# Optimization experiments

Hardware: AMD Instinct MI355X
Metric: run time of the kernel (lower is better)

Reference implementation:

```python
import jax, jax.numpy as jnp
import numpy as np

S, N, D, H = 1024, 8, 1024, 16
DK = D // H
SCALE = np.sqrt(DK).astype(np.float32)


def setup_inputs() -> dict:
    key = jax.random.key(0)
    ks = jax.random.split(key, 16)
    f32 = jnp.float32
    Qpoi = jax.random.normal(ks[0], (S, N, D), f32)
    Qsvi = jax.random.normal(ks[1], (S, N, D), f32)
    K = jax.random.normal(ks[2], (S, N, D), f32)
    V = jax.random.normal(ks[3], (S, N, D), f32)
    # padding mask: True = masked key; random valid lengths in [S//2, S]
    lengths = jax.random.randint(ks[4], (N,), S // 2, S + 1)
    key_padding_mask = jnp.arange(S)[None, :] >= lengths[:, None]  # [N, S] bool
    w = 0.02
    wq_poi_w = jax.random.normal(ks[5], (D, D), f32) * w
    wq_poi_b = jnp.zeros((D,), f32)
    wq_svi_w = jax.random.normal(ks[6], (D, D), f32) * w
    wq_svi_b = jnp.zeros((D,), f32)
    wk_w = jax.random.normal(ks[7], (D, D), f32) * w
    wk_b = jnp.zeros((D,), f32)
    wv_w = jax.random.normal(ks[8], (D, D), f32) * w
    wv_b = jnp.zeros((D,), f32)
    fc_w = jax.random.normal(ks[9], (D, D), f32) * w
    fc_b = jnp.zeros((D,), f32)
    return dict(Qpoi=Qpoi, Qsvi=Qsvi, K=K, V=V, key_padding_mask=key_padding_mask,
                wq_poi_w=wq_poi_w, wq_poi_b=wq_poi_b, wq_svi_w=wq_svi_w, wq_svi_b=wq_svi_b,
                wk_w=wk_w, wk_b=wk_b, wv_w=wv_w, wv_b=wv_b, fc_w=fc_w, fc_b=fc_b)


def _proj_heads(x, W, b):
    # x: [S, N, D] -> linear -> [N, H, S, DK]
    y = x @ W.T + b                      # [S, N, D]
    y = jnp.transpose(y, (1, 0, 2))      # [N, S, D]
    y = y.reshape(N, S, H, DK)
    return jnp.transpose(y, (0, 2, 1, 3))  # [N, H, S, DK]


def _attend(Qh, Kh, Vh, mask):
    # Qh,Kh,Vh: [N, H, S, DK]; mask: [N, S] bool (True = masked)
    scores = jnp.einsum('nhqd,nhkd->nhqk', Qh, Kh) / SCALE
    scores = jnp.where(mask[:, None, None, :], -jnp.inf, scores)
    attn = jax.nn.softmax(scores, axis=-1)  # dropout is identity in eval
    out = jnp.einsum('nhqk,nhkd->nhqd', attn, Vh)
    out = jnp.transpose(out, (0, 2, 1, 3)).reshape(N, S, D)  # [N, S, D]
    return out


def reference(Qpoi, Qsvi, K, V, key_padding_mask,
              wq_poi_w, wq_poi_b, wq_svi_w, wq_svi_b,
              wk_w, wk_b, wv_w, wv_b, fc_w, fc_b):
    Qp = _proj_heads(Qpoi, wq_poi_w, wq_poi_b)
    Qs = _proj_heads(Qsvi, wq_svi_w, wq_svi_b)
    Kh = _proj_heads(K, wk_w, wk_b)
    Vh = _proj_heads(V, wv_w, wv_b)
    poi = _attend(Qp, Kh, Vh, key_padding_mask)
    svi = _attend(Qs, Kh, Vh, key_padding_mask)
    poi_out = jnp.transpose(poi @ fc_w.T + fc_b, (1, 0, 2))  # [S, N, D]
    svi_out = jnp.transpose(svi @ fc_w.T + fc_b, (1, 0, 2))
    return (poi_out, svi_out)
```

## Files before the change

### kernel.cpp

```cpp
#include <hip/hip_runtime.h>

typedef unsigned short u16;
typedef unsigned int u32;
typedef short bf16x8 __attribute__((ext_vector_type(8)));
typedef float f32x4 __attribute__((ext_vector_type(4)));

__device__ __forceinline__ u16 f2bf(float f) {
  union { float f; u32 i; } v; v.f = f;
  u32 x = v.i;
  return (u16)((x + 0x7fffu + ((x >> 16) & 1u)) >> 16);
}

union Pack16 { u16 h[16]; float4 f4[2]; };

__device__ __forceinline__ void gld16(const u16* g, u16* l) {
  __builtin_amdgcn_global_load_lds((const __attribute__((address_space(1))) u32*)g,
                                   (__attribute__((address_space(3))) u32*)l, 16, 0, 0);
}

struct C2 { const float* s[2]; u16* d[2]; };
__global__ __launch_bounds__(256) void conv2_kernel(C2 c) {
  const int z = blockIdx.z;
  const size_t i = (size_t)blockIdx.x * 256 + threadIdx.x;
  const float4* s = (const float4*)c.s[z] + i * 2;
  float4 a = s[0], b = s[1];
  union { u16 h[8]; float4 f; } o;
  o.h[0] = f2bf(a.x); o.h[1] = f2bf(a.y); o.h[2] = f2bf(a.z); o.h[3] = f2bf(a.w);
  o.h[4] = f2bf(b.x); o.h[5] = f2bf(b.y); o.h[6] = f2bf(b.z); o.h[7] = f2bf(b.w);
  *(float4*)(c.d[z] + i * 8) = o.f;
}

struct W5 { const float* p[5]; };
__global__ __launch_bounds__(256) void conv_w_kernel(W5 w, u16* __restrict__ dst) {
  const int m = blockIdx.x >> 9;
  const size_t i = (size_t)(blockIdx.x & 511) * 256 + threadIdx.x;
  const float4* s = (const float4*)w.p[m] + i * 2;
  float4 a = s[0], b = s[1];
  union { u16 h[8]; float4 f; } o;
  o.h[0] = f2bf(a.x); o.h[1] = f2bf(a.y); o.h[2] = f2bf(a.z); o.h[3] = f2bf(a.w);
  o.h[4] = f2bf(b.x); o.h[5] = f2bf(b.y); o.h[6] = f2bf(b.z); o.h[7] = f2bf(b.w);
  *(float4*)(dst + ((size_t)m << 20) + i * 8) = o.f;
}

template<int ASRC>
__device__ __forceinline__ const u16* aAddr(const u16* A, int row, int k) {
  if constexpr (ASRC == 0) {
    return A + (size_t)row * 1024 + k;
  } else {
    const int n = row >> 10, s = row & 1023, h = k >> 6;
    return A + ((size_t)((n * 16 + h) * 1024 + s)) * 64 + (k & 63);
  }
}

struct GB { const void* A[2]; const void* W[2]; const float* bias[2]; void* out[2]; };

template<int MODEA, int MODEB, int ASRC, int WBF>
__global__ __launch_bounds__(256, 2) void gemm_bt(GB gb) {
  __shared__ __align__(16) u16 At[2][128 * 32];
  __shared__ __align__(16) u16 Bt[2][128 * 32];

  const int z = blockIdx.z;
  const u16* Ab = (const u16*)gb.A[z];
  const u16* Wb = (const u16*)gb.W[z];
  const float* bias = gb.bias[z];
  void* outv = gb.out[z];
  const int mode = z ? MODEB : MODEA;

  const int tid = threadIdx.x;
  const int lane = tid & 63, wave = tid >> 6;
  const int quad = lane >> 4, l16 = lane & 15;
  const int bm = blockIdx.y * 128, bn = blockIdx.x * 128;
  const int wm = (wave >> 1) * 64, wn = (wave & 1) * 64;

  const int r0 = wave * 32;
  const int lrow = lane >> 2;
  const int lk = (lane & 3) * 8;
  (void)lrow;

  const int srow = tid >> 1, scol = (tid & 1) * 16;

  f32x4 acc[4][4];
#pragma unroll
  for (int i = 0; i < 4; i++)
#pragma unroll
    for (int j = 0; j < 4; j++) acc[i][j] = (f32x4){0.f, 0.f, 0.f, 0.f};

  float4 wf[4];

  auto loadWf = [&](int k0) {
    const float* wp = (const float*)Wb + (size_t)(bn + srow) * 1024 + k0 + scol;
#pragma unroll
    for (int q = 0; q < 4; q++) wf[q] = ((const float4*)wp)[q];
  };
  auto stageA = [&](int b, int k0) {
    const int row = bm + r0 + (lane >> 2);
    gld16(aAddr<ASRC>(Ab, row, k0 + lk), At[b] + r0 * 32);
    gld16(aAddr<ASRC>(Ab, row + 16, k0 + lk), At[b] + (r0 + 16) * 32);
  };
  auto stageW = [&](int b, int k0) {
    if constexpr (WBF) {
      const int row = bn + r0 + (lane >> 2);
      gld16(Wb + (size_t)row * 1024 + k0 + lk, Bt[b] + r0 * 32);
      gld16(Wb + (size_t)(row + 16) * 1024 + k0 + lk, Bt[b] + (r0 + 16) * 32);
    } else {
      Pack16 pb;
#pragma unroll
      for (int q = 0; q < 4; q++) {
        pb.h[q * 4 + 0] = f2bf(wf[q].x);
        pb.h[q * 4 + 1] = f2bf(wf[q].y);
        pb.h[q * 4 + 2] = f2bf(wf[q].z);
        pb.h[q * 4 + 3] = f2bf(wf[q].w);
      }
      *(float4*)(Bt[b] + srow * 32 + scol) = pb.f4[0];
      *(float4*)(Bt[b] + srow * 32 + scol + 8) = pb.f4[1];
    }
  };

  if constexpr (!WBF) loadWf(0);
  stageA(0, 0);
  stageW(0, 0);
  if constexpr (!WBF) loadWf(32);

  for (int t = 0; t < 32; ++t) {
    const int cb = t & 1, nb = cb ^ 1;
    __syncthreads();
    if (t + 1 < 32) {
      stageA(nb, (t + 1) * 32);
      stageW(nb, (t + 1) * 32);
      if constexpr (!WBF) if (t + 2 < 32) loadWf((t + 2) * 32);
    }

    bf16x8 af[4], bfr[4];
#pragma unroll
    for (int mt = 0; mt < 4; mt++)
      af[mt] = *(const bf16x8*)(At[cb] + (wm + mt * 16 + l16) * 32 + quad * 8);
#pragma unroll
    for (int nt = 0; nt < 4; nt++)
      bfr[nt] = *(const bf16x8*)(Bt[cb] + (wn + nt * 16 + l16) * 32 + quad * 8);
#pragma unroll
    for (int mt = 0; mt < 4; mt++)
#pragma unroll
      for (int nt = 0; nt < 4; nt++)
        acc[mt][nt] = __builtin_amdgcn_mfma_f32_16x16x32_bf16(af[mt], bfr[nt], acc[mt][nt], 0, 0, 0);
  }

#pragma unroll
  for (int mt = 0; mt < 4; mt++) {
#pragma unroll
    for (int nt = 0; nt < 4; nt++) {
      const int col = bn + wn + nt * 16 + l16;
      const float bv = bias[col];
#pragma unroll
      for (int i = 0; i < 4; i++) {
        const int row = bm + wm + mt * 16 + quad * 4 + i;
        const float v = acc[mt][nt][i] + bv;
        if (mode == 0) {
          const int s = row >> 3, n = row & 7;
          const int h = col >> 6, dk = col & 63;
          ((u16*)outv)[(size_t)(((n * 16 + h) * 1024 + s) * 64 + dk)] = f2bf(v);
        } else if (mode == 1) {
          const int n = row >> 10, s = row & 1023;
          ((float*)outv)[(size_t)((s * 8 + n) * 1024 + col)] = v;
        } else {
          const int s = row >> 3, n = row & 7;
          const int h = col >> 6, dk = col & 63;
          ((u16*)outv)[(size_t)(((n * 16 + h) * 64 + dk) * 1024 + s)] = f2bf(v);
        }
      }
    }
  }
}

__global__ __launch_bounds__(256, 2) void attn2_kernel(const u16* __restrict__ Qs_g,
                                                       const u16* __restrict__ Qp_g,
                                                       const u16* __restrict__ K,
                                                       const u16* __restrict__ Vt_g,
                                                       const int* __restrict__ mask,
                                                       u16* __restrict__ OUTs,
                                                       u16* __restrict__ OUTp) {
  __shared__ __align__(16) u16 Ks[64 * 72];
  __shared__ __align__(16) u16 Vt[64 * 64];
  __shared__ __align__(16) u16 PsS[4 * 16 * 72];
  __shared__ __align__(16) u16 PsP[4 * 16 * 72];
  __shared__ float mbias[64];

  const int tid = threadIdx.x;
  const int lane = tid & 63, wave = tid >> 6;
  const int quad = lane >> 4, l16 = lane & 15;
  const int qt = blockIdx.x, nh = blockIdx.y;
  const int n = nh >> 4;
  const size_t base = (size_t)nh << 16;

  const int q0 = qt * 64 + wave * 16;
  bf16x8 qS0, qS1, qP0, qP1;
  {
    const u16* qp = Qs_g + base + (size_t)(q0 + l16) * 64 + quad * 8;
    qS0 = *(const bf16x8*)qp;
    qS1 = *(const bf16x8*)(qp + 32);
    const u16* qq = Qp_g + base + (size_t)(q0 + l16) * 64 + quad * 8;
    qP0 = *(const bf16x8*)qq;
    qP1 = *(const bf16x8*)(qq + 32);
  }

  float mS[4], mP[4];
  f32x4 oS[4], oP[4], lS, lP;
#pragma unroll
  for (int i = 0; i < 4; i++) { mS[i] = -1e30f; mP[i] = -1e30f; }
#pragma unroll
  for (int d = 0; d < 4; d++) { oS[d] = (f32x4){0.f, 0.f, 0.f, 0.f}; oP[d] = (f32x4){0.f, 0.f, 0.f, 0.f}; }
  lS = (f32x4){0.f, 0.f, 0.f, 0.f};
  lP = (f32x4){0.f, 0.f, 0.f, 0.f};

  bf16x8 vbOnes;
  {
    const short ob = (l16 == 0) ? (short)0x3F80 : (short)0;
#pragma unroll
    for (int j = 0; j < 8; j++) vbOnes[j] = ob;
  }

  const int sr = tid >> 2;
  const int sc = (tid & 3) * 16;
  const u16* kbase = K + base + (size_t)sr * 64 + sc;
  const u16* vbase = Vt_g + base + (size_t)sr * 1024 + sc;
  u16* vdst0 = Vt + sr * 64 + ((((sc >> 3) + 0) ^ (sr & 7)) << 3);
  u16* vdst1 = Vt + sr * 64 + ((((sc >> 3) + 1) ^ (sr & 7)) << 3);
  u16* pwS = PsS + wave * (16 * 72);
  u16* pwP = PsP + wave * (16 * 72);

  float4 kv0 = *(const float4*)(kbase);
  float4 kv1 = *(const float4*)(kbase + 8);
  float4 vv0 = *(const float4*)(vbase);
  float4 vv1 = *(const float4*)(vbase + 8);
  int mk = (tid < 64) ? mask[n * 1024 + tid] : 0;

  for (int kt = 0; kt < 16; kt++) {
    __syncthreads();
    *(float4*)(Ks + sr * 72 + sc) = kv0;
    *(float4*)(Ks + sr * 72 + sc + 8) = kv1;
    *(float4*)vdst0 = vv0;
    *(float4*)vdst1 = vv1;
    if (tid < 64) mbias[tid] = mk ? -1e30f : 0.0f;
    __syncthreads();

    if (kt + 1 < 16) {
      kv0 = *(const float4*)(kbase + (kt + 1) * 64 * 64);
      kv1 = *(const float4*)(kbase + (kt + 1) * 64 * 64 + 8);
      vv0 = *(const float4*)(vbase + (kt + 1) * 64);
      vv1 = *(const float4*)(vbase + (kt + 1) * 64 + 8);
      mk = (tid < 64) ? mask[n * 1024 + (kt + 1) * 64 + tid] : 0;
    }

    f32x4 sS[4], sP[4];
#pragma unroll
    for (int nt = 0; nt < 4; nt++) {
      bf16x8 b0 = *(const bf16x8*)(Ks + (nt * 16 + l16) * 72 + quad * 8);
      bf16x8 b1 = *(const bf16x8*)(Ks + (nt * 16 + l16) * 72 + 32 + quad * 8);
      f32x4 a = (f32x4){0.f, 0.f, 0.f, 0.f};
      a = __builtin_amdgcn_mfma_f32_16x16x32_bf16(qS0, b0, a, 0, 0, 0);
      a = __builtin_amdgcn_mfma_f32_16x16x32_bf16(qS1, b1, a, 0, 0, 0);
      sS[nt] = a;
      f32x4 c = (f32x4){0.f, 0.f, 0.f, 0.f};
      c = __builtin_amdgcn_mfma_f32_16x16x32_bf16(qP0, b0, c, 0, 0, 0);
      c = __builtin_amdgcn_mfma_f32_16x16x32_bf16(qP1, b1, c, 0, 0, 0);
      sP[nt] = c;
    }
    float mb[4];
#pragma unroll
    for (int nt = 0; nt < 4; nt++) mb[nt] = mbias[nt * 16 + l16];
#pragma unroll
    for (int nt = 0; nt < 4; nt++)
#pragma unroll
      for (int i = 0; i < 4; i++) {
        sS[nt][i] = sS[nt][i] * 0.125f + mb[nt];
        sP[nt][i] = sP[nt][i] * 0.125f + mb[nt];
      }

#pragma unroll
    for (int i = 0; i < 4; i++) {
      float m = fmaxf(fmaxf(sS[0][i], sS[1][i]), fmaxf(sS[2][i], sS[3][i]));
#pragma unroll
      for (int off = 1; off < 16; off <<= 1) m = fmaxf(m, __shfl_xor(m, off, 64));
      float mn = fmaxf(mS[i], m);
      float alpha = __expf(mS[i] - mn);
      mS[i] = mn;
#pragma unroll
      for (int d = 0; d < 4; d++) oS[d][i] *= alpha;
      lS[i] *= alpha;
    }
#pragma unroll
    for (int i = 0; i < 4; i++) {
      float m = fmaxf(fmaxf(sP[0][i], sP[1][i]), fmaxf(sP[2][i], sP[3][i]));
#pragma unroll
      for (int off = 1; off < 16; off <<= 1) m = fmaxf(m, __shfl_xor(m, off, 64));
      float mn = fmaxf(mP[i], m);
      float alpha = __expf(mP[i] - mn);
      mP[i] = mn;
#pragma unroll
      for (int d = 0; d < 4; d++) oP[d][i] *= alpha;
      lP[i] *= alpha;
    }
#pragma unroll
    for (int nt = 0; nt < 4; nt++)
#pragma unroll
      for (int i = 0; i < 4; i++) {
        pwS[(quad * 4 + i) * 72 + nt * 16 + l16] = f2bf(__expf(sS[nt][i] - mS[i]));
        pwP[(quad * 4 + i) * 72 + nt * 16 + l16] = f2bf(__expf(sP[nt][i] - mP[i]));
      }
    __syncthreads();

#pragma unroll
    for (int ks = 0; ks < 2; ks++) {
      bf16x8 paS = *(const bf16x8*)(pwS + l16 * 72 + ks * 32 + quad * 8);
      bf16x8 paP = *(const bf16x8*)(pwP + l16 * 72 + ks * 32 + quad * 8);
      lS = __builtin_amdgcn_mfma_f32_16x16x32_bf16(paS, vbOnes, lS, 0, 0, 0);
      lP = __builtin_amdgcn_mfma_f32_16x16x32_bf16(paP, vbOnes, lP, 0, 0, 0);
#pragma unroll
      for (int d = 0; d < 4; d++) {
        bf16x8 vb = *(const bf16x8*)(Vt + (d * 16 + l16) * 64 +
                                     (((ks * 4 + quad) ^ (l16 & 7)) << 3));
        oS[d] = __builtin_amdgcn_mfma_f32_16x16x32_bf16(paS, vb, oS[d], 0, 0, 0);
        oP[d] = __builtin_amdgcn_mfma_f32_16x16x32_bf16(paP, vb, oP[d], 0, 0, 0);
      }
    }
  }

#pragma unroll
  for (int i = 0; i < 4; i++) {
    const float lsv = __shfl(lS[i], lane & 48, 64);
    const float lpv = __shfl(lP[i], lane & 48, 64);
    const float invS = 1.0f / lsv;
    const float invP = 1.0f / lpv;
    const int q = q0 + quad * 4 + i;
    const size_t ob = base + (size_t)q * 64;
#pragma unroll
    for (int d = 0; d < 4; d++) {
      OUTs[ob + d * 16 + l16] = f2bf(oS[d][i] * invS);
      OUTp[ob + d * 16 + l16] = f2bf(oP[d][i] * invP);
    }
  }
}

extern "C" void kernel_launch(void* const* d_in, const int* in_sizes, int n_in,
                              void* d_out, int out_size, void* d_ws, size_t ws_size,
                              hipStream_t stream) {
  const float* Qpoi = (const float*)d_in[0];
  const float* Qsvi = (const float*)d_in[1];
  const float* Kin  = (const float*)d_in[2];
  const float* Vin  = (const float*)d_in[3];
  const int* mask   = (const int*)d_in[4];
  const float* wq_poi_w = (const float*)d_in[5];
  const float* wq_poi_b = (const float*)d_in[6];
  const float* wq_svi_w = (const float*)d_in[7];
  const float* wq_svi_b = (const float*)d_in[8];
  const float* wk_w = (const float*)d_in[9];
  const float* wk_b = (const float*)d_in[10];
  const float* wv_w = (const float*)d_in[11];
  const float* wv_b = (const float*)d_in[12];
  const float* fc_w = (const float*)d_in[13];
  const float* fc_b = (const float*)d_in[14];

  const size_t SZ = (size_t)8 * 16 * 1024 * 64;
  const size_t WBE = (size_t)5 << 20;
  u16* W0 = (u16*)d_ws;
  u16* W1 = W0 + SZ;
  u16* Wp = W1 + SZ;
  const bool haveWb = ws_size >= (2 * SZ + WBE) * sizeof(u16);

  float* Of = (float*)d_out;
  u16* R0 = (u16*)d_out;
  u16* R1 = R0 + SZ;
  u16* R2 = R0 + 2 * SZ;
  u16* R3 = R0 + 3 * SZ;

  dim3 bb(256, 1, 1);
  dim3 gg(8, 64, 2);
  dim3 ga(16, 128);
  dim3 gc(4096, 1, 2);

  if (haveWb) {
    W5 w5{{wk_w, wv_w, wq_svi_w, wq_poi_w, fc_w}};
    hipLaunchKernelGGL(conv_w_kernel, dim3(2560), bb, 0, stream, w5, Wp);
  }
  const u16* Wk  = Wp + ((size_t)0 << 20);
  const u16* Wv  = Wp + ((size_t)1 << 20);
  const u16* Wqs = Wp + ((size_t)2 << 20);
  const u16* Wqp = Wp + ((size_t)3 << 20);
  const u16* Wfc = Wp + ((size_t)4 << 20);

  {
    C2 c{{Kin, Vin}, {R0, R1}};
    hipLaunchKernelGGL(conv2_kernel, gc, bb, 0, stream, c);
    GB g{{R0, R1},
         {haveWb ? (const void*)Wk : (const void*)wk_w, haveWb ? (const void*)Wv : (const void*)wv_w},
         {wk_b, wv_b}, {(void*)W0, (void*)W1}};
    if (haveWb) hipLaunchKernelGGL((gemm_bt<0, 2, 0, 1>), gg, bb, 0, stream, g);
    else        hipLaunchKernelGGL((gemm_bt<0, 2, 0, 0>), gg, bb, 0, stream, g);
  }

  {
    C2 c{{Qsvi, Qpoi}, {R0, R1}};
    hipLaunchKernelGGL(conv2_kernel, gc, bb, 0, stream, c);
    GB g{{R0, R1},
         {haveWb ? (const void*)Wqs : (const void*)wq_svi_w, haveWb ? (const void*)Wqp : (const void*)wq_poi_w},
         {wq_svi_b, wq_poi_b}, {(void*)R2, (void*)R3}};
    if (haveWb) hipLaunchKernelGGL((gemm_bt<0, 0, 0, 1>), gg, bb, 0, stream, g);
    else        hipLaunchKernelGGL((gemm_bt<0, 0, 0, 0>), gg, bb, 0, stream, g);
  }

  hipLaunchKernelGGL(attn2_kernel, ga, bb, 0, stream,
                     (const u16*)R2, (const u16*)R3, (const u16*)W0, (const u16*)W1,
                     mask, R2, R3);

  hipMemcpyAsync(W0, R3, SZ * sizeof(u16), hipMemcpyDeviceToDevice, stream);
  hipMemcpyAsync(W1, R2, SZ * sizeof(u16), hipMemcpyDeviceToDevice, stream);
  {
    GB g{{W0, W1},
         {haveWb ? (const void*)Wfc : (const void*)fc_w, haveWb ? (const void*)Wfc : (const void*)fc_w},
         {fc_b, fc_b}, {(void*)Of, (void*)(Of + SZ)}};
    if (haveWb) hipLaunchKernelGGL((gemm_bt<1, 1, 1, 1>), gg, bb, 0, stream, g);
    else        hipLaunchKernelGGL((gemm_bt<1, 1, 1, 0>), gg, bb, 0, stream, g);
  }
}
```

Baseline: 572.2 us.

## Transpose score MFMA, lazy softmax rescale, packed bf16 P, drop ctx memcpys

The attention kernel now computes transposed score tiles (K as the A operand), so each lane holds a single query column. This turns the row max into two cross-quad shuffles. Rescaling of the running output is skipped unless the tile max exceeds the running max by more than 8, the row sum is accumulated in VALU instead of an extra ones-MFMA, and P is written to a swizzled LDS buffer with packed bf16 converts, dropping a __syncthreads. When workspace is large enough, attention writes its context into dedicated buffers so the two device-to-device memcpys before the output GEMM are avoided. The risks are a larger workspace requirement and possible fp32 headroom issues from the lazy rescale threshold.

Result: faster. 474.0 us (-17.2%).

```diff
diff --git a/kernel.cpp b/kernel.cpp
--- a/kernel.cpp
+++ b/kernel.cpp
@@ -9,6 +9,12 @@
   union { float f; u32 i; } v; v.f = f;
   u32 x = v.i;
   return (u16)((x + 0x7fffu + ((x >> 16) & 1u)) >> 16);
+}
+
+__device__ __forceinline__ u32 cvtpk_bf16(float a, float b) {
+  u32 r;
+  asm("v_cvt_pk_bf16_f32 %0, %1, %2" : "=v"(r) : "v"(a), "v"(b));
+  return r;
 }
 
 union Pack16 { u16 h[16]; float4 f4[2]; };
@@ -73,9 +79,7 @@
   const int wm = (wave >> 1) * 64, wn = (wave & 1) * 64;
 
   const int r0 = wave * 32;
-  const int lrow = lane >> 2;
   const int lk = (lane & 3) * 8;
-  (void)lrow;
 
   const int srow = tid >> 1, scol = (tid & 1) * 16;
 
@@ -180,8 +184,7 @@
                                                        u16* __restrict__ OUTp) {
   __shared__ __align__(16) u16 Ks[64 * 72];
   __shared__ __align__(16) u16 Vt[64 * 64];
-  __shared__ __align__(16) u16 PsS[4 * 16 * 72];
-  __shared__ __align__(16) u16 PsP[4 * 16 * 72];
+  __shared__ __align__(16) u16 Ps[4][2][1024];
   __shared__ float mbias[64];
 
   const int tid = threadIdx.x;
@@ -202,21 +205,10 @@
     qP1 = *(const bf16x8*)(qq + 32);
   }
 
-  float mS[4], mP[4];
-  f32x4 oS[4], oP[4], lS, lP;
-#pragma unroll
-  for (int i = 0; i < 4; i++) { mS[i] = -1e30f; mP[i] = -1e30f; }
+  float mS = -1e30f, mP = -1e30f, lS = 0.f, lP = 0.f;
+  f32x4 oS[4], oP[4];
 #pragma unroll
   for (int d = 0; d < 4; d++) { oS[d] = (f32x4){0.f, 0.f, 0.f, 0.f}; oP[d] = (f32x4){0.f, 0.f, 0.f, 0.f}; }
-  lS = (f32x4){0.f, 0.f, 0.f, 0.f};
-  lP = (f32x4){0.f, 0.f, 0.f, 0.f};
-
-  bf16x8 vbOnes;
-  {
-    const short ob = (l16 == 0) ? (short)0x3F80 : (short)0;
-#pragma unroll
-    for (int j = 0; j < 8; j++) vbOnes[j] = ob;
-  }
 
   const int sr = tid >> 2;
   const int sc = (tid & 3) * 16;
@@ -224,8 +216,8 @@
   const u16* vbase = Vt_g + base + (size_t)sr * 1024 + sc;
   u16* vdst0 = Vt + sr * 64 + ((((sc >> 3) + 0) ^ (sr & 7)) << 3);
   u16* vdst1 = Vt + sr * 64 + ((((sc >> 3) + 1) ^ (sr & 7)) << 3);
-  u16* pwS = PsS + wave * (16 * 72);
-  u16* pwP = PsP + wave * (16 * 72);
+  u16* psS = &Ps[wave][0][0];
+  u16* psP = &Ps[wave][1][0];
 
   float4 kv0 = *(const float4*)(kbase);
   float4 kv1 = *(const float4*)(kbase + 8);
@@ -256,64 +248,79 @@
       bf16x8 b0 = *(const bf16x8*)(Ks + (nt * 16 + l16) * 72 + quad * 8);
       bf16x8 b1 = *(const bf16x8*)(Ks + (nt * 16 + l16) * 72 + 32 + quad * 8);
       f32x4 a = (f32x4){0.f, 0.f, 0.f, 0.f};
-      a = __builtin_amdgcn_mfma_f32_16x16x32_bf16(qS0, b0, a, 0, 0, 0);
-      a = __builtin_amdgcn_mfma_f32_16x16x32_bf16(qS1, b1, a, 0, 0, 0);
+      a = __builtin_amdgcn_mfma_f32_16x16x32_bf16(b0, qS0, a, 0, 0, 0);
+      a = __builtin_amdgcn_mfma_f32_16x16x32_bf16(b1, qS1, a, 0, 0, 0);
       sS[nt] = a;
       f32x4 c = (f32x4){0.f, 0.f, 0.f, 0.f};
-      c = __builtin_amdgcn_mfma_f32_16x16x32_bf16(qP0, b0, c, 0, 0, 0);
-      c = __builtin_amdgcn_mfma_f32_16x16x32_bf16(qP1, b1, c, 0, 0, 0);
+      c = __builtin_amdgcn_mfma_f32_16x16x32_bf16(b0, qP0, c, 0, 0, 0);
+      c = __builtin_amdgcn_mfma_f32_16x16x32_bf16(b1, qP1, c, 0, 0, 0);
       sP[nt] = c;
     }
-    float mb[4];
-#pragma unroll
-    for (int nt = 0; nt < 4; nt++) mb[nt] = mbias[nt * 16 + l16];
 #pragma unroll
     for (int nt = 0; nt < 4; nt++)
 #pragma unroll
       for (int i = 0; i < 4; i++) {
-        sS[nt][i] = sS[nt][i] * 0.125f + mb[nt];
-        sP[nt][i] = sP[nt][i] * 0.125f + mb[nt];
+        const float mb = mbias[nt * 16 + quad * 4 + i];
+        sS[nt][i] = sS[nt][i] * 0.125f + mb;
+        sP[nt][i] = sP[nt][i] * 0.125f + mb;
       }
 
-#pragma unroll
-    for (int i = 0; i < 4; i++) {
-      float m = fmaxf(fmaxf(sS[0][i], sS[1][i]), fmaxf(sS[2][i], sS[3][i]));
-#pragma unroll
-      for (int off = 1; off < 16; off <<= 1) m = fmaxf(m, __shfl_xor(m, off, 64));
-      float mn = fmaxf(mS[i], m);
-      float alpha = __expf(mS[i] - mn);
-      mS[i] = mn;
-#pragma unroll
-      for (int d = 0; d < 4; d++) oS[d][i] *= alpha;
-      lS[i] *= alpha;
-    }
-#pragma unroll
-    for (int i = 0; i < 4; i++) {
-      float m = fmaxf(fmaxf(sP[0][i], sP[1][i]), fmaxf(sP[2][i], sP[3][i]));
-#pragma unroll
-      for (int off = 1; off < 16; off <<= 1) m = fmaxf(m, __shfl_xor(m, off, 64));
-      float mn = fmaxf(mP[i], m);
-      float alpha = __expf(mP[i] - mn);
-      mP[i] = mn;
-#pragma unroll
-      for (int d = 0; d < 4; d++) oP[d][i] *= alpha;
-      lP[i] *= alpha;
-    }
+    float mlS = sS[0][0], mlP = sP[0][0];
 #pragma unroll
     for (int nt = 0; nt < 4; nt++)
 #pragma unroll
       for (int i = 0; i < 4; i++) {
-        pwS[(quad * 4 + i) * 72 + nt * 16 + l16] = f2bf(__expf(sS[nt][i] - mS[i]));
-        pwP[(quad * 4 + i) * 72 + nt * 16 + l16] = f2bf(__expf(sP[nt][i] - mP[i]));
+        if (nt || i) { mlS = fmaxf(mlS, sS[nt][i]); mlP = fmaxf(mlP, sP[nt][i]); }
       }
-    __syncthreads();
+    mlS = fmaxf(mlS, __shfl_xor(mlS, 16, 64));
+    mlS = fmaxf(mlS, __shfl_xor(mlS, 32, 64));
+    mlP = fmaxf(mlP, __shfl_xor(mlP, 16, 64));
+    mlP = fmaxf(mlP, __shfl_xor(mlP, 32, 64));
+
+    if (!__all(mlS - mS <= 8.0f)) {
+      const float mn = fmaxf(mS, mlS);
+      const float al = __expf(mS - mn);
+      mS = mn; lS *= al;
+      float a0 = __shfl(al, quad * 4 + 0, 64), a1 = __shfl(al, quad * 4 + 1, 64);
+      float a2 = __shfl(al, quad * 4 + 2, 64), a3 = __shfl(al, quad * 4 + 3, 64);
+#pragma unroll
+      for (int d = 0; d < 4; d++) { oS[d][0] *= a0; oS[d][1] *= a1; oS[d][2] *= a2; oS[d][3] *= a3; }
+    }
+    if (!__all(mlP - mP <= 8.0f)) {
+      const float mn = fmaxf(mP, mlP);
+      const float al = __expf(mP - mn);
+      mP = mn; lP *= al;
+      float a0 = __shfl(al, quad * 4 + 0, 64), a1 = __shfl(al, quad * 4 + 1, 64);
+      float a2 = __shfl(al, quad * 4 + 2, 64), a3 = __shfl(al, quad * 4 + 3, 64);
+#pragma unroll
+      for (int d = 0; d < 4; d++) { oP[d][0] *= a0; oP[d][1] *= a1; oP[d][2] *= a2; oP[d][3] *= a3; }
+    }
+
+    float lsS = 0.f, lsP = 0.f;
+#pragma unroll
+    for (int nt = 0; nt < 4; nt++) {
+      const int woff = l16 * 64 + (((2 * nt + (quad >> 1)) ^ (l16 & 7)) << 3) + ((quad & 1) << 2);
+      float p0 = __expf(sS[nt][0] - mS), p1 = __expf(sS[nt][1] - mS);
+      float p2 = __expf(sS[nt][2] - mS), p3 = __expf(sS[nt][3] - mS);
+      lsS += (p0 + p1) + (p2 + p3);
+      uint2 w; w.x = cvtpk_bf16(p0, p1); w.y = cvtpk_bf16(p2, p3);
+      *(uint2*)(psS + woff) = w;
+      p0 = __expf(sP[nt][0] - mP); p1 = __expf(sP[nt][1] - mP);
+      p2 = __expf(sP[nt][2] - mP); p3 = __expf(sP[nt][3] - mP);
+      lsP += (p0 + p1) + (p2 + p3);
+      uint2 u; u.x = cvtpk_bf16(p0, p1); u.y = cvtpk_bf16(p2, p3);
+      *(uint2*)(psP + woff) = u;
+    }
+    lsS += __shfl_xor(lsS, 16, 64); lsS += __shfl_xor(lsS, 32, 64);
+    lsP += __shfl_xor(lsP, 16, 64); lsP += __shfl_xor(lsP, 32, 64);
+    lS += lsS;
+    lP += lsP;
 
 #pragma unroll
     for (int ks = 0; ks < 2; ks++) {
-      bf16x8 paS = *(const bf16x8*)(pwS + l16 * 72 + ks * 32 + quad * 8);
-      bf16x8 paP = *(const bf16x8*)(pwP + l16 * 72 + ks * 32 + quad * 8);
-      lS = __builtin_amdgcn_mfma_f32_16x16x32_bf16(paS, vbOnes, lS, 0, 0, 0);
-      lP = __builtin_amdgcn_mfma_f32_16x16x32_bf16(paP, vbOnes, lP, 0, 0, 0);
+      const int roff = l16 * 64 + ((((ks * 4 + quad) ^ (l16 & 7))) << 3);
+      bf16x8 paS = *(const bf16x8*)(psS + roff);
+      bf16x8 paP = *(const bf16x8*)(psP + roff);
 #pragma unroll
       for (int d = 0; d < 4; d++) {
         bf16x8 vb = *(const bf16x8*)(Vt + (d * 16 + l16) * 64 +
@@ -324,12 +331,16 @@
     }
   }
 
+  float liS[4], liP[4];
 #pragma unroll
   for (int i = 0; i < 4; i++) {
-    const float lsv = __shfl(lS[i], lane & 48, 64);
-    const float lpv = __shfl(lP[i], lane & 48, 64);
-    const float invS = 1.0f / lsv;
-    const float invP = 1.0f / lpv;
+    liS[i] = __shfl(lS, quad * 4 + i, 64);
+    liP[i] = __shfl(lP, quad * 4 + i, 64);
+  }
+#pragma unroll
+  for (int i = 0; i < 4; i++) {
+    const float invS = 1.0f / liS[i];
+    const float invP = 1.0f / liP[i];
     const int q = q0 + quad * 4 + i;
     const size_t ob = base + (size_t)q * 64;
 #pragma unroll
@@ -364,7 +375,11 @@
   u16* W0 = (u16*)d_ws;
   u16* W1 = W0 + SZ;
   u16* Wp = W1 + SZ;
+  u16* W2 = Wp + WBE;
+  u16* W3 = W2 + SZ;
   const bool haveWb = ws_size >= (2 * SZ + WBE) * sizeof(u16);
+  const bool haveW2 = ws_size >= (3 * SZ + WBE) * sizeof(u16);
+  const bool haveW3 = ws_size >= (4 * SZ + WBE) * sizeof(u16);
 
   float* Of = (float*)d_out;
   u16* R0 = (u16*)d_out;
@@ -407,14 +422,20 @@
     else        hipLaunchKernelGGL((gemm_bt<0, 0, 0, 0>), gg, bb, 0, stream, g);
   }
 
+  u16* ctxS = (haveWb && haveW2) ? W2 : R2;
+  u16* ctxP = (haveWb && haveW3) ? W3 : R3;
   hipLaunchKernelGGL(attn2_kernel, ga, bb, 0, stream,
                      (const u16*)R2, (const u16*)R3, (const u16*)W0, (const u16*)W1,
-                     mask, R2, R3);
-
-  hipMemcpyAsync(W0, R3, SZ * sizeof(u16), hipMemcpyDeviceToDevice, stream);
-  hipMemcpyAsync(W1, R2, SZ * sizeof(u16), hipMemcpyDeviceToDevice, stream);
+                     mask, ctxS, ctxP);
+
+  const u16* Ap;
+  const u16* As;
+  if (haveWb && haveW3) { Ap = W3; }
+  else { hipMemcpyAsync(W0, ctxP, SZ * sizeof(u16), hipMemcpyDeviceToDevice, stream); Ap = W0; }
+  if (haveWb && haveW2) { As = W2; }
+  else { hipMemcpyAsync(W1, ctxS, SZ * sizeof(u16), hipMemcpyDeviceToDevice, stream); As = W1; }
   {
-    GB g{{W0, W1},
+    GB g{{Ap, As},
          {haveWb ? (const void*)Wfc : (const void*)fc_w, haveWb ? (const void*)Wfc : (const void*)fc_w},
          {fc_b, fc_b}, {(void*)Of, (void*)(Of + SZ)}};
     if (haveWb) hipLaunchKernelGGL((gemm_bt<1, 1, 1, 1>), gg, bb, 0, stream, g);
```
